# Optimization experiments

Hardware: AMD Instinct MI355X
Metric: run time of the kernel (lower is better)

Reference implementation:

```python
import jax, jax.numpy as jnp
import numpy as np

B, D, C = 8192, 64, 2048
BETA = 0.25
EPS = 1e-6


def setup_inputs() -> dict:
    key = jax.random.key(0)
    k1, k2, k3 = jax.random.split(key, 3)
    x = jax.random.normal(k1, (B, D), dtype=jnp.float32)
    prev_q = jax.random.normal(k2, (B, D), dtype=jnp.float32)
    codes = jax.random.normal(k3, (1, C, D), dtype=jnp.float32) * 0.1  # learned codebook param
    return {"x": x, "prev_q": prev_q, "codes": codes}


def _rotation_matrix(u, v, eps=EPS):
    # u: (B, D) unit vectors, v: (D,) unit vector. Rodrigues-like rotation mapping v -> u.
    uvT = u[:, :, None] * v[None, None, :]          # (B, D, D)
    vuT = v[None, :, None] * u[:, None, :]          # (B, D, D)
    A = uvT - vuT
    A2 = jnp.einsum('bij,bjk->bik', A, A)
    dot = jnp.sum(u * v[None, :], axis=-1)[:, None, None]  # (B,1,1)
    I = jnp.eye(u.shape[-1], dtype=u.dtype)
    return I[None] + A + A2 / (1.0 + dot + eps)


def reference(x, prev_q, codes):
    # F.normalize(prev_q, dim=-1, eps=1e-6)
    norm = jnp.linalg.norm(prev_q, axis=-1, keepdims=True)
    u = prev_q / jnp.maximum(norm, EPS)
    v = jnp.full((D,), 1.0 / float(D) ** 0.5, dtype=x.dtype)  # registered buffer v

    R = _rotation_matrix(u, v)                      # (B, D, D); R_inv = R^T
    x_canonical = jnp.einsum('bij,bi->bj', R, x)    # R^T @ x

    c0 = codes[0]                                   # (C, D)
    # squared L2 distances (B, C) via GEMM expansion (same math as sum((x-c)^2))
    dists = (jnp.sum(x_canonical ** 2, axis=-1, keepdims=True)
             - 2.0 * (x_canonical @ c0.T)
             + jnp.sum(c0 ** 2, axis=-1)[None, :])
    indices = jnp.argmin(dists, axis=-1)            # (B,)
    quantized_canonical = c0[indices]               # (B, D)

    # STE: value equals quantized_canonical, gradient flows to x_canonical
    q_out = x_canonical + jax.lax.stop_gradient(quantized_canonical - x_canonical)
    quantized = jnp.einsum('bij,bj->bi', R, q_out)  # R @ q_out

    loss_commit = jnp.mean(jnp.sum((x - jax.lax.stop_gradient(quantized_canonical)) ** 2, axis=-1))
    loss_codebook = jnp.mean(jnp.sum((jax.lax.stop_gradient(x) - quantized_canonical) ** 2, axis=-1))
    loss = loss_commit + BETA * loss_codebook
    return quantized, indices, loss
```

## Files before the change

kernel.cpp:

```cpp
#include <hip/hip_runtime.h>
#include <math.h>

#define B_ROWS 8192
#define DIM 64
#define NCODES 2048
#define NSPLIT 16
#define CODES_PER_SPLIT (NCODES / NSPLIT)
#define TILES_PER_WAVE (CODES_PER_SPLIT / 16)
#define EPSF 1e-6f
#define BETA 0.25f
#define V_VAL 0.125f

typedef __attribute__((ext_vector_type(8))) short sh8;
typedef __attribute__((ext_vector_type(4))) float f32x4;

__device__ __forceinline__ float wave_sum64(float v) {
#pragma unroll
    for (int m = 32; m >= 1; m >>= 1) v += __shfl_xor(v, m, 64);
    return v;
}

__device__ __forceinline__ unsigned short f2bf(float f) {
    unsigned u = __float_as_uint(f);
    unsigned r = (u + 0x7fffu + ((u >> 16) & 1u)) >> 16;
    return (unsigned short)r;
}
__device__ __forceinline__ float bf2f(unsigned short h) {
    return __uint_as_float(((unsigned)h) << 16);
}


__global__ void rq_prep_codes(const float* __restrict__ codes,
                              float* __restrict__ cn,
                              unsigned short* __restrict__ cfrag) {
    int tid = threadIdx.x;
    int lane = tid & 63;
    int c = blockIdx.x * 4 + (tid >> 6);
    float cv = codes[(size_t)c * DIM + lane];
    float s = wave_sum64(cv * cv);
    if (lane == 0) cn[c] = s;

    unsigned short s0 = f2bf(cv);
    float r = cv - bf2f(s0);
    unsigned short s1 = f2bf(r);
    r -= bf2f(s1);
    unsigned short s2 = f2bf(r);

    int ct = c >> 4, m = c & 15;
    int h = lane >> 5, q = (lane >> 3) & 3, j = lane & 7;
    int lanep = q * 16 + m;
    size_t base = ((size_t)(ct * 3) * 2 + h) * 512 + (size_t)lanep * 8 + j;
    cfrag[base] = s0;
    cfrag[base + 2 * 512] = s1;
    cfrag[base + 4 * 512] = s2;
}

__global__ void rq_prep_rows(const float* __restrict__ x,
                             const float* __restrict__ pq,
                             unsigned short* __restrict__ xfrag,
                             float* __restrict__ uo,
                             float* __restrict__ duv) {
    int tid = threadIdx.x;
    int lane = tid & 63;
    int r = blockIdx.x * 4 + (tid >> 6);
    float xv = x[(size_t)r * DIM + lane];
    float qv = pq[(size_t)r * DIM + lane];
    float n2 = wave_sum64(qv * qv);
    float inv = 1.0f / fmaxf(sqrtf(n2), EPSF);
    float uv = qv * inv;
    float d = V_VAL * wave_sum64(uv);
    float a = wave_sum64(uv * xv);
    float b = V_VAL * wave_sum64(xv);
    float den = 1.0f + d + EPSF;
    float cu = -b + (d * b - a) / den;
    float cv = a - (b - d * a) / den;
    float xcv = xv + uv * cu + V_VAL * cv;

    uo[(size_t)r * DIM + lane] = uv;
    if (lane == 0) duv[r] = d;

    unsigned short s0 = f2bf(xcv);
    float rr = xcv - bf2f(s0);
    unsigned short s1 = f2bf(rr);
    rr -= bf2f(s1);
    unsigned short s2 = f2bf(rr);

    int rt = r >> 4, m = r & 15;
    int h = lane >> 5, q = (lane >> 3) & 3, j = lane & 7;
    int lanep = q * 16 + m;
    size_t base = ((size_t)(rt * 3) * 2 + h) * 512 + (size_t)lanep * 8 + j;
    xfrag[base] = s0;
    xfrag[base + 2 * 512] = s1;
    xfrag[base + 4 * 512] = s2;
}

__global__ __launch_bounds__(256) void rq_dist_mfma(
        const unsigned short* __restrict__ xfrag,
        const unsigned short* __restrict__ cfrag,
        const float* __restrict__ cn,
        float* __restrict__ pd,
        int* __restrict__ pi) {
    int tid = threadIdx.x;
    int lane = tid & 63;
    int w = tid >> 6;
    int rb = blockIdx.x >> 4;
    int cs = blockIdx.x & (NSPLIT - 1);
    int r0 = rb * 128 + w * 32;
    int rt0 = r0 >> 4;

    const sh8* xf = (const sh8*)xfrag;
    const sh8* cf = (const sh8*)cfrag;

    sh8 afr[2][3][2];
#pragma unroll
    for (int rs = 0; rs < 2; ++rs)
#pragma unroll
        for (int s = 0; s < 3; ++s)
#pragma unroll
            for (int h = 0; h < 2; ++h)
                afr[rs][s][h] = xf[(size_t)(((rt0 + rs) * 3 + s) * 2 + h) * 64 + lane];

    float bv0[4], bv1[4];
    int bi0[4], bi1[4];
#pragma unroll
    for (int i = 0; i < 4; ++i) {
        bv0[i] = INFINITY; bv1[i] = INFINITY;
        bi0[i] = 0x7fffffff; bi1[i] = 0x7fffffff;
    }

    int cbase = cs * CODES_PER_SPLIT;
    for (int t = 0; t < TILES_PER_WAVE; ++t) {
        int c0 = cbase + t * 16;
        int ct = c0 >> 4;
        sh8 bfr[3][2];
#pragma unroll
        for (int s = 0; s < 3; ++s)
#pragma unroll
            for (int h = 0; h < 2; ++h)
                bfr[s][h] = cf[(size_t)((ct * 3 + s) * 2 + h) * 64 + lane];

        f32x4 acc0 = {0.f, 0.f, 0.f, 0.f};
        f32x4 acc1 = {0.f, 0.f, 0.f, 0.f};
#pragma unroll
        for (int h = 0; h < 2; ++h) {
            acc0 = __builtin_amdgcn_mfma_f32_16x16x32_bf16(afr[0][2][h], bfr[0][h], acc0, 0, 0, 0);
            acc0 = __builtin_amdgcn_mfma_f32_16x16x32_bf16(afr[0][1][h], bfr[1][h], acc0, 0, 0, 0);
            acc0 = __builtin_amdgcn_mfma_f32_16x16x32_bf16(afr[0][0][h], bfr[2][h], acc0, 0, 0, 0);
            acc0 = __builtin_amdgcn_mfma_f32_16x16x32_bf16(afr[0][1][h], bfr[0][h], acc0, 0, 0, 0);
            acc0 = __builtin_amdgcn_mfma_f32_16x16x32_bf16(afr[0][0][h], bfr[1][h], acc0, 0, 0, 0);
            acc0 = __builtin_amdgcn_mfma_f32_16x16x32_bf16(afr[0][0][h], bfr[0][h], acc0, 0, 0, 0);

            acc1 = __builtin_amdgcn_mfma_f32_16x16x32_bf16(afr[1][2][h], bfr[0][h], acc1, 0, 0, 0);
            acc1 = __builtin_amdgcn_mfma_f32_16x16x32_bf16(afr[1][1][h], bfr[1][h], acc1, 0, 0, 0);
            acc1 = __builtin_amdgcn_mfma_f32_16x16x32_bf16(afr[1][0][h], bfr[2][h], acc1, 0, 0, 0);
            acc1 = __builtin_amdgcn_mfma_f32_16x16x32_bf16(afr[1][1][h], bfr[0][h], acc1, 0, 0, 0);
            acc1 = __builtin_amdgcn_mfma_f32_16x16x32_bf16(afr[1][0][h], bfr[1][h], acc1, 0, 0, 0);
            acc1 = __builtin_amdgcn_mfma_f32_16x16x32_bf16(afr[1][0][h], bfr[0][h], acc1, 0, 0, 0);
        }

        float cnv = cn[c0 + (lane & 15)];
        int idxv = c0 + (lane & 15);
#pragma unroll
        for (int reg = 0; reg < 4; ++reg) {
            float s0 = fmaf(-2.0f, acc0[reg], cnv);
            if (s0 < bv0[reg]) { bv0[reg] = s0; bi0[reg] = idxv; }
            float s1 = fmaf(-2.0f, acc1[reg], cnv);
            if (s1 < bv1[reg]) { bv1[reg] = s1; bi1[reg] = idxv; }
        }
    }

#pragma unroll
    for (int rs = 0; rs < 2; ++rs) {
#pragma unroll
        for (int reg = 0; reg < 4; ++reg) {
            float v = rs ? bv1[reg] : bv0[reg];
            int ix = rs ? bi1[reg] : bi0[reg];
#pragma unroll
            for (int m = 1; m < 16; m <<= 1) {
                float ov = __shfl_xor(v, m, 64);
                int oi = __shfl_xor(ix, m, 64);
                if (ov < v || (ov == v && oi < ix)) { v = ov; ix = oi; }
            }
            int row = r0 + rs * 16 + (lane >> 4) * 4 + reg;
            if ((lane & 15) == reg) {
                pd[(size_t)cs * B_ROWS + row] = v;
                pi[(size_t)cs * B_ROWS + row] = ix;
            }
        }
    }
}

__global__ void rq_epilogue(const float* __restrict__ x,
                            const float* __restrict__ codes,
                            const float* __restrict__ uo,
                            const float* __restrict__ duv,
                            const float* __restrict__ pd,
                            const int* __restrict__ pi,
                            float* __restrict__ out_q,
                            float* __restrict__ out_idx,
                            float* __restrict__ lossbuf) {
    int tid = threadIdx.x;
    int lane = tid & 63;
    int r = blockIdx.x * 4 + (tid >> 6);

    float dmin = INFINITY;
    int imin = 0x7fffffff;
    if (lane < NSPLIT) {
        dmin = pd[(size_t)lane * B_ROWS + r];
        imin = pi[(size_t)lane * B_ROWS + r];
    }
#pragma unroll
    for (int m = 1; m < 64; m <<= 1) {
        float od = __shfl_xor(dmin, m, 64);
        int oi = __shfl_xor(imin, m, 64);
        if (od < dmin || (od == dmin && oi < imin)) { dmin = od; imin = oi; }
    }
    int idx = imin;

    float qc = codes[(size_t)idx * DIM + lane];
    float uv = uo[(size_t)r * DIM + lane];
    float xv = x[(size_t)r * DIM + lane];
    float d = duv[r];

    float aq = wave_sum64(uv * qc);
    float bq = V_VAL * wave_sum64(qc);
    float den = 1.0f + d + EPSF;
    float cu = bq + (d * bq - aq) / den;
    float cv = -aq - (bq - d * aq) / den;
    float qout = qc + uv * cu + V_VAL * cv;
    out_q[(size_t)r * DIM + lane] = qout;

    float diff = xv - qc;
    float l = wave_sum64(diff * diff);
    if (lane == 0) {
        out_idx[r] = (float)idx;
        lossbuf[r] = l;
    }
}

__global__ void rq_loss_reduce(const float* __restrict__ lossbuf,
                               float* __restrict__ out_loss) {
    __shared__ float part[16];
    int tid = threadIdx.x;
    float s = 0.f;
#pragma unroll
    for (int i = 0; i < B_ROWS / 1024; ++i) s += lossbuf[tid + i * 1024];
    s = wave_sum64(s);
    if ((tid & 63) == 0) part[tid >> 6] = s;
    __syncthreads();
    if (tid < 64) {
        float v = (tid < 16) ? part[tid] : 0.f;
        v = wave_sum64(v);
        if (tid == 0) *out_loss = v * (1.0f + BETA) * (1.0f / (float)B_ROWS);
    }
}

extern "C" void kernel_launch(void* const* d_in, const int* in_sizes, int n_in,
                              void* d_out, int out_size, void* d_ws, size_t ws_size,
                              hipStream_t stream) {
    const float* x     = (const float*)d_in[0];
    const float* pq    = (const float*)d_in[1];
    const float* codes = (const float*)d_in[2];

    float* out      = (float*)d_out;
    float* out_q    = out;
    float* out_idx  = out + (size_t)B_ROWS * DIM;
    float* out_loss = out_idx + B_ROWS;

    char* ws = (char*)d_ws;
    const size_t MB = 1024 * 1024;
    float* uo            = (float*)ws;
    float* duv           = (float*)(ws + 2 * MB);
    float* cn            = (float*)(ws + 2 * MB + 64 * 1024);
    unsigned short* xfrg = (unsigned short*)(ws + 3 * MB);
    unsigned short* cfrg = (unsigned short*)(ws + 6 * MB);
    float* pd            = (float*)(ws + 7 * MB);
    int*   pi            = (int*)(ws + 7 * MB + 512 * 1024);
    float* lbuf          = (float*)(ws + 8 * MB);

    rq_prep_codes<<<NCODES / 4, 256, 0, stream>>>(codes, cn, cfrg);
    rq_prep_rows<<<B_ROWS / 4, 256, 0, stream>>>(x, pq, xfrg, uo, duv);
    rq_dist_mfma<<<64 * NSPLIT, 256, 0, stream>>>(xfrg, cfrg, cn, pd, pi);
    rq_epilogue<<<B_ROWS / 4, 256, 0, stream>>>(
        x, codes, uo, duv, pd, pi, out_q, out_idx, lbuf);
    rq_loss_reduce<<<1, 1024, 0, stream>>>(lbuf, out_loss);
}
```

Baseline: 92.99 us.

## Fuse prep kernels and fold epilogue into distance kernel via last-block counter

Merges the codebook and row preparation kernels into one launch, and folds the argmin merge, output reconstruction and loss reduction into the distance kernel. The last of the 16 split blocks for each row block, detected with an atomic counter, does the epilogue. Partial results are now stored row-major so each row's 16 candidates sit next to each other. This cuts five launches to two and drops the loss buffer pass. In exchange the epilogue runs serially in only 64 blocks, and the loss is summed with float atomics, so its order is nondeterministic.

```diff
diff --git a/kernel.cpp b/kernel.cpp
--- a/kernel.cpp
+++ b/kernel.cpp
@@ -7,6 +7,7 @@
 #define NSPLIT 16
 #define CODES_PER_SPLIT (NCODES / NSPLIT)
 #define TILES_PER_WAVE (CODES_PER_SPLIT / 16)
+#define NRB (B_ROWS / 128)
 #define EPSF 1e-6f
 #define BETA 0.25f
 #define V_VAL 0.125f
@@ -29,77 +30,84 @@
     return __uint_as_float(((unsigned)h) << 16);
 }
 
-
-__global__ void rq_prep_codes(const float* __restrict__ codes,
-                              float* __restrict__ cn,
-                              unsigned short* __restrict__ cfrag) {
-    int tid = threadIdx.x;
-    int lane = tid & 63;
-    int c = blockIdx.x * 4 + (tid >> 6);
-    float cv = codes[(size_t)c * DIM + lane];
-    float s = wave_sum64(cv * cv);
-    if (lane == 0) cn[c] = s;
-
-    unsigned short s0 = f2bf(cv);
-    float r = cv - bf2f(s0);
+__device__ __forceinline__ void write_frag3(unsigned short* frag, int rc,
+                                            int dim, float val) {
+    unsigned short s0 = f2bf(val);
+    float r = val - bf2f(s0);
     unsigned short s1 = f2bf(r);
     r -= bf2f(s1);
     unsigned short s2 = f2bf(r);
-
-    int ct = c >> 4, m = c & 15;
-    int h = lane >> 5, q = (lane >> 3) & 3, j = lane & 7;
+    int t = rc >> 4, m = rc & 15;
+    int h = dim >> 5, q = (dim >> 3) & 3, j = dim & 7;
     int lanep = q * 16 + m;
-    size_t base = ((size_t)(ct * 3) * 2 + h) * 512 + (size_t)lanep * 8 + j;
-    cfrag[base] = s0;
-    cfrag[base + 2 * 512] = s1;
-    cfrag[base + 4 * 512] = s2;
-}
-
-__global__ void rq_prep_rows(const float* __restrict__ x,
-                             const float* __restrict__ pq,
-                             unsigned short* __restrict__ xfrag,
-                             float* __restrict__ uo,
-                             float* __restrict__ duv) {
+    size_t base = ((size_t)(t * 3) * 2 + h) * 512 + (size_t)lanep * 8 + j;
+    frag[base] = s0;
+    frag[base + 2 * 512] = s1;
+    frag[base + 4 * 512] = s2;
+}
+
+__global__ __launch_bounds__(256) void rq_prep(
+        const float* __restrict__ x,
+        const float* __restrict__ pq,
+        const float* __restrict__ codes,
+        float* __restrict__ cn,
+        unsigned short* __restrict__ cfrag,
+        unsigned short* __restrict__ xfrag,
+        float* __restrict__ uo,
+        float* __restrict__ duv,
+        int* __restrict__ cnt,
+        float* __restrict__ out_loss) {
     int tid = threadIdx.x;
     int lane = tid & 63;
-    int r = blockIdx.x * 4 + (tid >> 6);
-    float xv = x[(size_t)r * DIM + lane];
-    float qv = pq[(size_t)r * DIM + lane];
-    float n2 = wave_sum64(qv * qv);
-    float inv = 1.0f / fmaxf(sqrtf(n2), EPSF);
-    float uv = qv * inv;
-    float d = V_VAL * wave_sum64(uv);
-    float a = wave_sum64(uv * xv);
-    float b = V_VAL * wave_sum64(xv);
-    float den = 1.0f + d + EPSF;
-    float cu = -b + (d * b - a) / den;
-    float cv = a - (b - d * a) / den;
-    float xcv = xv + uv * cu + V_VAL * cv;
-
-    uo[(size_t)r * DIM + lane] = uv;
-    if (lane == 0) duv[r] = d;
-
-    unsigned short s0 = f2bf(xcv);
-    float rr = xcv - bf2f(s0);
-    unsigned short s1 = f2bf(rr);
-    rr -= bf2f(s1);
-    unsigned short s2 = f2bf(rr);
-
-    int rt = r >> 4, m = r & 15;
-    int h = lane >> 5, q = (lane >> 3) & 3, j = lane & 7;
-    int lanep = q * 16 + m;
-    size_t base = ((size_t)(rt * 3) * 2 + h) * 512 + (size_t)lanep * 8 + j;
-    xfrag[base] = s0;
-    xfrag[base + 2 * 512] = s1;
-    xfrag[base + 4 * 512] = s2;
-}
-
-__global__ __launch_bounds__(256) void rq_dist_mfma(
+    int w = tid >> 6;
+
+    if (blockIdx.x < NCODES / 4) {
+        int c = blockIdx.x * 4 + w;
+        float cv = codes[(size_t)c * DIM + lane];
+        float s = wave_sum64(cv * cv);
+        if (lane == 0) cn[c] = s;
+        write_frag3(cfrag, c, lane, cv);
+        if (blockIdx.x == 0) {
+            if (tid < NRB) cnt[tid] = 0;
+            if (tid == NRB) *out_loss = 0.0f;
+        }
+    } else {
+        int r = (blockIdx.x - NCODES / 4) * 4 + w;
+        float xv = x[(size_t)r * DIM + lane];
+        float qv = pq[(size_t)r * DIM + lane];
+        float n2 = wave_sum64(qv * qv);
+        float inv = 1.0f / fmaxf(sqrtf(n2), EPSF);
+        float uv = qv * inv;
+        float d = V_VAL * wave_sum64(uv);
+        float a = wave_sum64(uv * xv);
+        float b = V_VAL * wave_sum64(xv);
+        float den = 1.0f + d + EPSF;
+        float cu = -b + (d * b - a) / den;
+        float cv = a - (b - d * a) / den;
+        float xcv = xv + uv * cu + V_VAL * cv;
+        uo[(size_t)r * DIM + lane] = uv;
+        if (lane == 0) duv[r] = d;
+        write_frag3(xfrag, r, lane, xcv);
+    }
+}
+
+__global__ __launch_bounds__(256) void rq_dist_fused(
         const unsigned short* __restrict__ xfrag,
         const unsigned short* __restrict__ cfrag,
         const float* __restrict__ cn,
+        const float* __restrict__ codes,
+        const float* __restrict__ uo,
+        const float* __restrict__ duv,
+        const float* __restrict__ x,
         float* __restrict__ pd,
-        int* __restrict__ pi) {
+        int* __restrict__ pi,
+        int* __restrict__ cnt,
+        float* __restrict__ out_q,
+        float* __restrict__ out_idx,
+        float* __restrict__ out_loss) {
+    __shared__ int s_flag;
+    __shared__ float s_part[4];
+
     int tid = threadIdx.x;
     int lane = tid & 63;
     int w = tid >> 6;
@@ -183,75 +191,61 @@
             }
             int row = r0 + rs * 16 + (lane >> 4) * 4 + reg;
             if ((lane & 15) == reg) {
-                pd[(size_t)cs * B_ROWS + row] = v;
-                pi[(size_t)cs * B_ROWS + row] = ix;
+                pd[(size_t)row * NSPLIT + cs] = v;
+                pi[(size_t)row * NSPLIT + cs] = ix;
             }
         }
     }
-}
-
-__global__ void rq_epilogue(const float* __restrict__ x,
-                            const float* __restrict__ codes,
-                            const float* __restrict__ uo,
-                            const float* __restrict__ duv,
-                            const float* __restrict__ pd,
-                            const int* __restrict__ pi,
-                            float* __restrict__ out_q,
-                            float* __restrict__ out_idx,
-                            float* __restrict__ lossbuf) {
-    int tid = threadIdx.x;
-    int lane = tid & 63;
-    int r = blockIdx.x * 4 + (tid >> 6);
-
-    float dmin = INFINITY;
-    int imin = 0x7fffffff;
-    if (lane < NSPLIT) {
-        dmin = pd[(size_t)lane * B_ROWS + r];
-        imin = pi[(size_t)lane * B_ROWS + r];
-    }
-#pragma unroll
-    for (int m = 1; m < 64; m <<= 1) {
-        float od = __shfl_xor(dmin, m, 64);
-        int oi = __shfl_xor(imin, m, 64);
-        if (od < dmin || (od == dmin && oi < imin)) { dmin = od; imin = oi; }
-    }
-    int idx = imin;
-
-    float qc = codes[(size_t)idx * DIM + lane];
-    float uv = uo[(size_t)r * DIM + lane];
-    float xv = x[(size_t)r * DIM + lane];
-    float d = duv[r];
-
-    float aq = wave_sum64(uv * qc);
-    float bq = V_VAL * wave_sum64(qc);
-    float den = 1.0f + d + EPSF;
-    float cu = bq + (d * bq - aq) / den;
-    float cv = -aq - (bq - d * aq) / den;
-    float qout = qc + uv * cu + V_VAL * cv;
-    out_q[(size_t)r * DIM + lane] = qout;
-
-    float diff = xv - qc;
-    float l = wave_sum64(diff * diff);
-    if (lane == 0) {
-        out_idx[r] = (float)idx;
-        lossbuf[r] = l;
-    }
-}
-
-__global__ void rq_loss_reduce(const float* __restrict__ lossbuf,
-                               float* __restrict__ out_loss) {
-    __shared__ float part[16];
-    int tid = threadIdx.x;
-    float s = 0.f;
-#pragma unroll
-    for (int i = 0; i < B_ROWS / 1024; ++i) s += lossbuf[tid + i * 1024];
-    s = wave_sum64(s);
-    if ((tid & 63) == 0) part[tid >> 6] = s;
+
     __syncthreads();
-    if (tid < 64) {
-        float v = (tid < 16) ? part[tid] : 0.f;
-        v = wave_sum64(v);
-        if (tid == 0) *out_loss = v * (1.0f + BETA) * (1.0f / (float)B_ROWS);
+    if (tid == 0) {
+        __threadfence();
+        int old = atomicAdd(&cnt[rb], 1);
+        s_flag = (old == NSPLIT - 1) ? 1 : 0;
+    }
+    __syncthreads();
+    if (!s_flag) return;
+    __threadfence();
+
+    float lsum = 0.f;
+    for (int i = 0; i < 32; ++i) {
+        int row = rb * 128 + w * 32 + i;
+        float pv = INFINITY;
+        int iv = 0x7fffffff;
+        if (lane < NSPLIT) {
+            pv = pd[(size_t)row * NSPLIT + lane];
+            iv = pi[(size_t)row * NSPLIT + lane];
+        }
+#pragma unroll
+        for (int m = 1; m < NSPLIT; m <<= 1) {
+            float ov = __shfl_xor(pv, m, 64);
+            int oi = __shfl_xor(iv, m, 64);
+            if (ov < pv || (ov == pv && oi < iv)) { pv = ov; iv = oi; }
+        }
+        int idx = __shfl(iv, 0, 64);
+
+        float qc = codes[(size_t)idx * DIM + lane];
+        float uvv = uo[(size_t)row * DIM + lane];
+        float xv = x[(size_t)row * DIM + lane];
+        float dv = duv[row];
+
+        float aq = wave_sum64(uvv * qc);
+        float bq = V_VAL * wave_sum64(qc);
+        float den = 1.0f + dv + EPSF;
+        float cu = bq + (dv * bq - aq) / den;
+        float cw = -aq - (bq - dv * aq) / den;
+        out_q[(size_t)row * DIM + lane] = qc + uvv * cu + V_VAL * cw;
+
+        float diff = xv - qc;
+        lsum += diff * diff;
+        if (lane == 0) out_idx[row] = (float)idx;
+    }
+    lsum = wave_sum64(lsum);
+    if (lane == 0) s_part[w] = lsum;
+    __syncthreads();
+    if (tid == 0) {
+        float t = (s_part[0] + s_part[1]) + (s_part[2] + s_part[3]);
+        atomicAdd(out_loss, t * (1.0f + BETA) * (1.0f / (float)B_ROWS));
     }
 }
 
@@ -272,16 +266,15 @@
     float* uo            = (float*)ws;
     float* duv           = (float*)(ws + 2 * MB);
     float* cn            = (float*)(ws + 2 * MB + 64 * 1024);
+    int*   cnt           = (int*)(ws + 2 * MB + 128 * 1024);
     unsigned short* xfrg = (unsigned short*)(ws + 3 * MB);
     unsigned short* cfrg = (unsigned short*)(ws + 6 * MB);
     float* pd            = (float*)(ws + 7 * MB);
     int*   pi            = (int*)(ws + 7 * MB + 512 * 1024);
-    float* lbuf          = (float*)(ws + 8 * MB);
-
-    rq_prep_codes<<<NCODES / 4, 256, 0, stream>>>(codes, cn, cfrg);
-    rq_prep_rows<<<B_ROWS / 4, 256, 0, stream>>>(x, pq, xfrg, uo, duv);
-    rq_dist_mfma<<<64 * NSPLIT, 256, 0, stream>>>(xfrg, cfrg, cn, pd, pi);
-    rq_epilogue<<<B_ROWS / 4, 256, 0, stream>>>(
-        x, codes, uo, duv, pd, pi, out_q, out_idx, lbuf);
-    rq_loss_reduce<<<1, 1024, 0, stream>>>(lbuf, out_loss);
-}
+
+    rq_prep<<<NCODES / 4 + B_ROWS / 4, 256, 0, stream>>>(
+        x, pq, codes, cn, cfrg, xfrg, uo, duv, cnt, out_loss);
+    rq_dist_fused<<<NRB * NSPLIT, 256, 0, stream>>>(
+        xfrg, cfrg, cn, codes, uo, duv, x, pd, pi, cnt,
+        out_q, out_idx, out_loss);
+}
```

Result: slower. 225.1 us (+142.1%).
